# Kernel tuning notes

Hardware: AMD Instinct MI355X
Metric: run time of the kernel (lower is better)

## Reference

```python
import jax, jax.numpy as jnp
import numpy as np

K = 8  # avg_kernel (pool kernel == stride, and nearest-upsample factor)


def conv1x1(u, W, b):
    # 1x1 conv == per-pixel linear map over channels
    return jnp.einsum('bchw,oc->bohw', u, W) + b[None, :, None, None]


def setup_inputs() -> dict:
    key = jax.random.key(0)
    ks = jax.random.split(key, 9)
    C = 64
    x = jax.random.normal(ks[0], (8, C, 512, 512), dtype=jnp.float32)
    def w(k):
        return jax.random.normal(k, (C, C), dtype=jnp.float32) * 0.05
    def bias(k):
        return jax.random.normal(k, (C,), dtype=jnp.float32) * 0.05
    return {
        'x': x,
        'Wt': w(ks[1]), 'bt': bias(ks[2]),
        'Wp': w(ks[3]), 'bp': bias(ks[4]),
        'Wg': w(ks[5]), 'bg': bias(ks[6]),
        'Wc': w(ks[7]), 'bc': bias(ks[8]),
    }


def reference(x, Wt, bt, Wp, bp, Wg, bg, Wc, bc):
    B, C, H, W = x.shape
    # AvgPool2d(kernel=K, stride=K): exact reshape-mean since H,W divisible by K
    u = x.reshape(B, C, H // K, K, W // K, K).mean(axis=(3, 5))  # [B,C,h,w]
    b_, c_, h, w_ = u.shape
    N = h * w_
    theta = conv1x1(u, Wt, bt).reshape(B, C, N).transpose(0, 2, 1)  # [B,N,C]
    phi = conv1x1(u, Wp, bp).reshape(B, C, N)                       # [B,C,N] (downsample = flatten)
    g = conv1x1(u, Wg, bg).reshape(B, C, N).transpose(0, 2, 1)      # [B,N,C]
    attn = jax.nn.softmax(jnp.einsum('bnc,bcm->bnm', theta, phi), axis=-1)  # [B,N,N], unscaled
    y = jnp.einsum('bnm,bmc->bnc', attn, g)                         # [B,N,C]
    y = y.transpose(0, 2, 1).reshape(B, C, h, w_)
    y = conv1x1(y, Wc, bc)
    # F.interpolate(size=[H,W]) default nearest; integer factor K -> exact repeat
    y = jnp.repeat(jnp.repeat(y, K, axis=2), K, axis=3)
    return y
```

## Files before the change

kernel.cpp:

```cpp
#include <hip/hip_runtime.h>
#include <hip/hip_bf16.h>


typedef short short8 __attribute__((ext_vector_type(8)));
typedef float floatx4 __attribute__((ext_vector_type(4)));

__device__ inline unsigned short f2bf(float f) {
    union { float f; unsigned int u; } v; v.f = f;
    unsigned int u = v.u;
    u += 0x7fff + ((u >> 16) & 1);
    return (unsigned short)(u >> 16);
}

__device__ inline float rowsum16(float x) {
    x += __int_as_float(__builtin_amdgcn_update_dpp(0, __float_as_int(x), 0x121, 0xf, 0xf, false));
    x += __int_as_float(__builtin_amdgcn_update_dpp(0, __float_as_int(x), 0x122, 0xf, 0xf, false));
    x += __int_as_float(__builtin_amdgcn_update_dpp(0, __float_as_int(x), 0x124, 0xf, 0xf, false));
    x += __int_as_float(__builtin_amdgcn_update_dpp(0, __float_as_int(x), 0x128, 0xf, 0xf, false));
    return x;
}

__global__ __launch_bounds__(256) void k_pool(const float* __restrict__ x,
                                              float* __restrict__ u) {
    int id = blockIdx.x * 256 + threadIdx.x;
    int ow = id & 63;
    int oh = (id >> 6) & 63;
    int bc = id >> 12;
    const float* p = x + ((size_t)bc * 512 + oh * 8) * 512 + ow * 8;
    float s = 0.f;
#pragma unroll
    for (int r = 0; r < 8; ++r) {
        const float4* q = (const float4*)(p + r * 512);
        float4 a = q[0], b = q[1];
        s += a.x + a.y + a.z + a.w + b.x + b.y + b.z + b.w;
    }
    u[id] = s * (1.f / 64.f);
}

__global__ __launch_bounds__(256) void k_qkv(const float* __restrict__ u,
    const float* __restrict__ Wt, const float* __restrict__ bt,
    const float* __restrict__ Wp, const float* __restrict__ bp,
    const float* __restrict__ Wg, const float* __restrict__ bg,
    unsigned short* __restrict__ th, unsigned short* __restrict__ ph,
    unsigned short* __restrict__ gT) {
    __shared__ float U[64 * 68];
    int b = blockIdx.x >> 6;
    int n0 = (blockIdx.x & 63) * 64;
    int t = threadIdx.x;
    int lane = t & 63, wv = t >> 6;
#pragma unroll
    for (int i = 0; i < 4; ++i) {
        int f4 = t + 256 * i;
        int cin = f4 >> 4, pos = f4 & 15;
        float4 v = *(const float4*)(u + ((size_t)(b * 64 + cin)) * 4096 + n0 + pos * 4);
        U[(pos * 4 + 0) * 68 + cin] = v.x;
        U[(pos * 4 + 1) * 68 + cin] = v.y;
        U[(pos * 4 + 2) * 68 + cin] = v.z;
        U[(pos * 4 + 3) * 68 + cin] = v.w;
    }
    __syncthreads();
    float4 ur[16];
#pragma unroll
    for (int q = 0; q < 16; ++q) ur[q] = *(const float4*)&U[lane * 68 + q * 4];
    __syncthreads();
    unsigned* T = (unsigned*)U;
    int cb = __builtin_amdgcn_readfirstlane(wv * 16);
    size_t gbase = (size_t)(b * 64) * 4096 + n0 + lane;
    float atp = 0.f, app = 0.f;
#pragma unroll 2
    for (int i = 0; i < 16; ++i) {
        int cout = cb + i;
        const float* wt = Wt + cout * 64;
        const float* wp = Wp + cout * 64;
        const float* wg = Wg + cout * 64;
        float t0 = bt[cout], t1 = 0.f;
        float q0 = bp[cout], q1 = 0.f;
        float g0 = bg[cout], g1 = 0.f;
#pragma unroll
        for (int q = 0; q < 16; ++q) {
            float4 x = ur[q];
            if (q & 1) {
                t1 = fmaf(wt[4*q+3], x.w, fmaf(wt[4*q+2], x.z, fmaf(wt[4*q+1], x.y, fmaf(wt[4*q], x.x, t1))));
                q1 = fmaf(wp[4*q+3], x.w, fmaf(wp[4*q+2], x.z, fmaf(wp[4*q+1], x.y, fmaf(wp[4*q], x.x, q1))));
                g1 = fmaf(wg[4*q+3], x.w, fmaf(wg[4*q+2], x.z, fmaf(wg[4*q+1], x.y, fmaf(wg[4*q], x.x, g1))));
            } else {
                t0 = fmaf(wt[4*q+3], x.w, fmaf(wt[4*q+2], x.z, fmaf(wt[4*q+1], x.y, fmaf(wt[4*q], x.x, t0))));
                q0 = fmaf(wp[4*q+3], x.w, fmaf(wp[4*q+2], x.z, fmaf(wp[4*q+1], x.y, fmaf(wp[4*q], x.x, q0))));
                g0 = fmaf(wg[4*q+3], x.w, fmaf(wg[4*q+2], x.z, fmaf(wg[4*q+1], x.y, fmaf(wg[4*q], x.x, g0))));
            }
        }
        float at = t0 + t1, ap = q0 + q1, ag = g0 + g1;
        gT[gbase + (size_t)cout * 4096] = f2bf(ag);
        if (i & 1) {
            T[lane * 68 + wv * 8 + (i >> 1)]      = (unsigned)f2bf(atp) | ((unsigned)f2bf(at) << 16);
            T[lane * 68 + 32 + wv * 8 + (i >> 1)] = (unsigned)f2bf(app) | ((unsigned)f2bf(ap) << 16);
        } else { atp = at; app = ap; }
    }
    __syncthreads();
#pragma unroll
    for (int j = 0; j < 2; ++j) {
        int qi = t + 256 * j;
        int r = qi >> 3, c4 = qi & 7;
        uint4 vt = *(const uint4*)&T[r * 68 + c4 * 4];
        uint4 vp = *(const uint4*)&T[r * 68 + 32 + c4 * 4];
        size_t o = ((size_t)(b * 4096 + n0 + r)) * 64 + c4 * 8;
        *(uint4*)(th + o) = vt;
        *(uint4*)(ph + o) = vp;
    }
}

__global__ __launch_bounds__(256) void k_attn(
    const unsigned short* __restrict__ th,
    const unsigned short* __restrict__ ph,
    const unsigned short* __restrict__ gT,
    float* __restrict__ y) {
    __shared__ unsigned short Th[64 * 72];
    __shared__ unsigned short Ph[2][64 * 72];
    __shared__ unsigned short Gt[2][64 * 72];
    __shared__ unsigned short Pl[4 * 16 * 72];
    int b = blockIdx.x >> 6;
    int n0 = (blockIdx.x & 63) * 64;
    int t = threadIdx.x;
    int wave = t >> 6, lane = t & 63, quad = lane >> 4, l16 = lane & 15;
    int row = t >> 2, cg = t & 3;

    {
        const unsigned short* src = th + ((size_t)(b * 4096 + n0 + row)) * 64;
        *(short8*)(Th + row * 72 + cg * 8)      = *(const short8*)(src + cg * 8);
        *(short8*)(Th + row * 72 + 32 + cg * 8) = *(const short8*)(src + 32 + cg * 8);
        const unsigned short* sp = ph + ((size_t)(b * 4096 + row)) * 64;
        *(short8*)(Ph[0] + row * 72 + cg * 8)      = *(const short8*)(sp + cg * 8);
        *(short8*)(Ph[0] + row * 72 + 32 + cg * 8) = *(const short8*)(sp + 32 + cg * 8);
        const unsigned short* sg = gT + ((size_t)(b * 64 + row)) * 4096;
        *(short8*)(Gt[0] + row * 72 + cg * 8)      = *(const short8*)(sg + cg * 8);
        *(short8*)(Gt[0] + row * 72 + 32 + cg * 8) = *(const short8*)(sg + 32 + cg * 8);
    }
    __syncthreads();
    short8 a0 = *(const short8*)(Th + (wave * 16 + l16) * 72 + quad * 8);
    short8 a1 = *(const short8*)(Th + (wave * 16 + l16) * 72 + 32 + quad * 8);

    floatx4 Yacc[4];
#pragma unroll
    for (int ct = 0; ct < 4; ++ct) Yacc[ct] = (floatx4){0.f, 0.f, 0.f, 0.f};
    float l[4] = {0.f, 0.f, 0.f, 0.f};

    int cur = 0;
    for (int mt = 0; mt < 64; ++mt) {
        int mn = ((mt + 1) & 63) * 64;
        short8 r0, r1, r2, r3;
        {
            const unsigned short* sp = ph + ((size_t)(b * 4096 + mn + row)) * 64;
            r0 = *(const short8*)(sp + cg * 8);
            r1 = *(const short8*)(sp + 32 + cg * 8);
            const unsigned short* sg = gT + ((size_t)(b * 64 + row)) * 4096 + mn;
            r2 = *(const short8*)(sg + cg * 8);
            r3 = *(const short8*)(sg + 32 + cg * 8);
        }
        const unsigned short* PhC = Ph[cur];
        const unsigned short* GtC = Gt[cur];

        float psum[4] = {0.f, 0.f, 0.f, 0.f};
#pragma unroll
        for (int ct = 0; ct < 4; ++ct) {
            short8 b0 = *(const short8*)(PhC + (ct * 16 + l16) * 72 + quad * 8);
            short8 b1 = *(const short8*)(PhC + (ct * 16 + l16) * 72 + 32 + quad * 8);
            floatx4 acc = (floatx4){0.f, 0.f, 0.f, 0.f};
            __builtin_amdgcn_s_setprio(1);
            acc = __builtin_amdgcn_mfma_f32_16x16x32_bf16(a0, b0, acc, 0, 0, 0);
            acc = __builtin_amdgcn_mfma_f32_16x16x32_bf16(a1, b1, acc, 0, 0, 0);
            __builtin_amdgcn_s_setprio(0);
#pragma unroll
            for (int r = 0; r < 4; ++r) {
                float e = __expf(acc[r]);
                psum[r] += e;
                Pl[wave * 16 * 72 + (quad * 4 + r) * 72 + ct * 16 + l16] = f2bf(e);
            }
        }
#pragma unroll
        for (int r = 0; r < 4; ++r) l[r] += rowsum16(psum[r]);
        short8 p0 = *(const short8*)(Pl + wave * 16 * 72 + l16 * 72 + quad * 8);
        short8 p1 = *(const short8*)(Pl + wave * 16 * 72 + l16 * 72 + 32 + quad * 8);
        __builtin_amdgcn_s_setprio(1);
#pragma unroll
        for (int ct = 0; ct < 4; ++ct) {
            short8 g0 = *(const short8*)(GtC + (ct * 16 + l16) * 72 + quad * 8);
            short8 g1 = *(const short8*)(GtC + (ct * 16 + l16) * 72 + 32 + quad * 8);
            Yacc[ct] = __builtin_amdgcn_mfma_f32_16x16x32_bf16(p0, g0, Yacc[ct], 0, 0, 0);
            Yacc[ct] = __builtin_amdgcn_mfma_f32_16x16x32_bf16(p1, g1, Yacc[ct], 0, 0, 0);
        }
        __builtin_amdgcn_s_setprio(0);
        unsigned short* PhN = Ph[cur ^ 1];
        unsigned short* GtN = Gt[cur ^ 1];
        *(short8*)(PhN + row * 72 + cg * 8)      = r0;
        *(short8*)(PhN + row * 72 + 32 + cg * 8) = r1;
        *(short8*)(GtN + row * 72 + cg * 8)      = r2;
        *(short8*)(GtN + row * 72 + 32 + cg * 8) = r3;
        __syncthreads();
        cur ^= 1;
    }
#pragma unroll
    for (int ct = 0; ct < 4; ++ct)
#pragma unroll
        for (int r = 0; r < 4; ++r) {
            int rr = n0 + wave * 16 + quad * 4 + r;
            y[((size_t)(b * 4096 + rr)) * 64 + ct * 16 + l16] = Yacc[ct][r] / l[r];
        }
}

__global__ __launch_bounds__(256) void k_out(const float* __restrict__ y,
    const float* __restrict__ Wc, const float* __restrict__ bc,
    float* __restrict__ out) {
    __shared__ float Y[64 * 66];
    int b = blockIdx.x >> 6;
    int oh = blockIdx.x & 63;
    int t = threadIdx.x;
#pragma unroll
    for (int i = 0; i < 4; ++i) {
        int f4 = t + 256 * i;
        int w = f4 >> 4, cgp = f4 & 15;
        float4 v = *(const float4*)(y + ((size_t)(b * 4096 + oh * 64 + w)) * 64 + cgp * 4);
        Y[(cgp * 4 + 0) * 66 + w] = v.x;
        Y[(cgp * 4 + 1) * 66 + w] = v.y;
        Y[(cgp * 4 + 2) * 66 + w] = v.z;
        Y[(cgp * 4 + 3) * 66 + w] = v.w;
    }
    __syncthreads();
    int w = t & 63, wv = t >> 6;
#pragma unroll 2
    for (int i = 0; i < 16; ++i) {
        int c = wv + 4 * i;
        float acc = bc[c];
#pragma unroll
        for (int cin = 0; cin < 64; ++cin)
            acc += Wc[c * 64 + cin] * Y[cin * 66 + w];
        float4 v4 = {acc, acc, acc, acc};
        float* base = out + (((size_t)(b * 64 + c)) * 512 + oh * 8) * 512 + w * 8;
#pragma unroll
        for (int r = 0; r < 8; ++r) {
            *(float4*)(base + (size_t)r * 512) = v4;
            *(float4*)(base + (size_t)r * 512 + 4) = v4;
        }
    }
}

extern "C" void kernel_launch(void* const* d_in, const int* in_sizes, int n_in,
                              void* d_out, int out_size, void* d_ws, size_t ws_size,
                              hipStream_t stream) {
    const float* x  = (const float*)d_in[0];
    const float* Wt = (const float*)d_in[1];
    const float* bt = (const float*)d_in[2];
    const float* Wp = (const float*)d_in[3];
    const float* bp = (const float*)d_in[4];
    const float* Wg = (const float*)d_in[5];
    const float* bg = (const float*)d_in[6];
    const float* Wc = (const float*)d_in[7];
    const float* bc = (const float*)d_in[8];
    float* out = (float*)d_out;
    char* ws = (char*)d_ws;
    float* u            = (float*)(ws);
    unsigned short* th  = (unsigned short*)(ws + (8  << 20));
    unsigned short* ph  = (unsigned short*)(ws + (12 << 20));
    unsigned short* gT  = (unsigned short*)(ws + (16 << 20));
    float* y            = (float*)(ws + (20 << 20));

    hipLaunchKernelGGL(k_pool, dim3(8192), dim3(256), 0, stream, x, u);
    hipLaunchKernelGGL(k_qkv,  dim3(512),  dim3(256), 0, stream,
                       u, Wt, bt, Wp, bp, Wg, bg, th, ph, gT);
    hipLaunchKernelGGL(k_attn, dim3(512),  dim3(256), 0, stream, th, ph, gT, y);
    hipLaunchKernelGGL(k_out,  dim3(512),  dim3(256), 0, stream, y, Wc, bc, out);
}
```

Measured before the change: 1.234 ms.

## Double attention query rows per block to reuse K/V tiles across two row groups

Each attention block now handles 128 query rows instead of 64, with each wave owning two 16-row groups that share the same phi/g LDS tiles. Theta fragments are loaded directly from global into registers, removing the Th shared buffer. This halves the number of K/V tile loads and barriers per query row, but it also halves the grid to 256 blocks, which may leave some of the MI355X's compute units idle, and it raises register use.

```diff
diff --git a/kernel.cpp b/kernel.cpp
--- a/kernel.cpp
+++ b/kernel.cpp
@@ -114,20 +114,23 @@
     const unsigned short* __restrict__ ph,
     const unsigned short* __restrict__ gT,
     float* __restrict__ y) {
-    __shared__ unsigned short Th[64 * 72];
     __shared__ unsigned short Ph[2][64 * 72];
     __shared__ unsigned short Gt[2][64 * 72];
-    __shared__ unsigned short Pl[4 * 16 * 72];
-    int b = blockIdx.x >> 6;
-    int n0 = (blockIdx.x & 63) * 64;
+    __shared__ unsigned short Pl[4][32 * 72];
+    int b = blockIdx.x >> 5;
+    int n0 = (blockIdx.x & 31) * 128;
     int t = threadIdx.x;
     int wave = t >> 6, lane = t & 63, quad = lane >> 4, l16 = lane & 15;
     int row = t >> 2, cg = t & 3;
 
+    short8 a[2][2];
+#pragma unroll
+    for (int rg = 0; rg < 2; ++rg) {
+        const unsigned short* src = th + ((size_t)(b * 4096 + n0 + wave * 32 + rg * 16 + l16)) * 64;
+        a[rg][0] = *(const short8*)(src + quad * 8);
+        a[rg][1] = *(const short8*)(src + 32 + quad * 8);
+    }
     {
-        const unsigned short* src = th + ((size_t)(b * 4096 + n0 + row)) * 64;
-        *(short8*)(Th + row * 72 + cg * 8)      = *(const short8*)(src + cg * 8);
-        *(short8*)(Th + row * 72 + 32 + cg * 8) = *(const short8*)(src + 32 + cg * 8);
         const unsigned short* sp = ph + ((size_t)(b * 4096 + row)) * 64;
         *(short8*)(Ph[0] + row * 72 + cg * 8)      = *(const short8*)(sp + cg * 8);
         *(short8*)(Ph[0] + row * 72 + 32 + cg * 8) = *(const short8*)(sp + 32 + cg * 8);
@@ -136,13 +139,13 @@
         *(short8*)(Gt[0] + row * 72 + 32 + cg * 8) = *(const short8*)(sg + 32 + cg * 8);
     }
     __syncthreads();
-    short8 a0 = *(const short8*)(Th + (wave * 16 + l16) * 72 + quad * 8);
-    short8 a1 = *(const short8*)(Th + (wave * 16 + l16) * 72 + 32 + quad * 8);
-
-    floatx4 Yacc[4];
-#pragma unroll
-    for (int ct = 0; ct < 4; ++ct) Yacc[ct] = (floatx4){0.f, 0.f, 0.f, 0.f};
-    float l[4] = {0.f, 0.f, 0.f, 0.f};
+
+    floatx4 Yacc[2][4];
+#pragma unroll
+    for (int rg = 0; rg < 2; ++rg)
+#pragma unroll
+        for (int ct = 0; ct < 4; ++ct) Yacc[rg][ct] = (floatx4){0.f, 0.f, 0.f, 0.f};
+    float l[2][4] = {{0.f,0.f,0.f,0.f},{0.f,0.f,0.f,0.f}};
 
     int cur = 0;
     for (int mt = 0; mt < 64; ++mt) {
@@ -159,34 +162,46 @@
         const unsigned short* PhC = Ph[cur];
         const unsigned short* GtC = Gt[cur];
 
-        float psum[4] = {0.f, 0.f, 0.f, 0.f};
+        float psum[2][4] = {{0.f,0.f,0.f,0.f},{0.f,0.f,0.f,0.f}};
 #pragma unroll
         for (int ct = 0; ct < 4; ++ct) {
             short8 b0 = *(const short8*)(PhC + (ct * 16 + l16) * 72 + quad * 8);
             short8 b1 = *(const short8*)(PhC + (ct * 16 + l16) * 72 + 32 + quad * 8);
-            floatx4 acc = (floatx4){0.f, 0.f, 0.f, 0.f};
-            __builtin_amdgcn_s_setprio(1);
-            acc = __builtin_amdgcn_mfma_f32_16x16x32_bf16(a0, b0, acc, 0, 0, 0);
-            acc = __builtin_amdgcn_mfma_f32_16x16x32_bf16(a1, b1, acc, 0, 0, 0);
-            __builtin_amdgcn_s_setprio(0);
-#pragma unroll
-            for (int r = 0; r < 4; ++r) {
-                float e = __expf(acc[r]);
-                psum[r] += e;
-                Pl[wave * 16 * 72 + (quad * 4 + r) * 72 + ct * 16 + l16] = f2bf(e);
-            }
-        }
-#pragma unroll
-        for (int r = 0; r < 4; ++r) l[r] += rowsum16(psum[r]);
-        short8 p0 = *(const short8*)(Pl + wave * 16 * 72 + l16 * 72 + quad * 8);
-        short8 p1 = *(const short8*)(Pl + wave * 16 * 72 + l16 * 72 + 32 + quad * 8);
+#pragma unroll
+            for (int rg = 0; rg < 2; ++rg) {
+                floatx4 acc = (floatx4){0.f, 0.f, 0.f, 0.f};
+                __builtin_amdgcn_s_setprio(1);
+                acc = __builtin_amdgcn_mfma_f32_16x16x32_bf16(a[rg][0], b0, acc, 0, 0, 0);
+                acc = __builtin_amdgcn_mfma_f32_16x16x32_bf16(a[rg][1], b1, acc, 0, 0, 0);
+                __builtin_amdgcn_s_setprio(0);
+#pragma unroll
+                for (int r = 0; r < 4; ++r) {
+                    float e = __expf(acc[r]);
+                    psum[rg][r] += e;
+                    Pl[wave][(rg * 16 + quad * 4 + r) * 72 + ct * 16 + l16] = f2bf(e);
+                }
+            }
+        }
+#pragma unroll
+        for (int rg = 0; rg < 2; ++rg)
+#pragma unroll
+            for (int r = 0; r < 4; ++r) l[rg][r] += rowsum16(psum[rg][r]);
+        short8 p[2][2];
+#pragma unroll
+        for (int rg = 0; rg < 2; ++rg) {
+            p[rg][0] = *(const short8*)(Pl[wave] + (rg * 16 + l16) * 72 + quad * 8);
+            p[rg][1] = *(const short8*)(Pl[wave] + (rg * 16 + l16) * 72 + 32 + quad * 8);
+        }
         __builtin_amdgcn_s_setprio(1);
 #pragma unroll
         for (int ct = 0; ct < 4; ++ct) {
             short8 g0 = *(const short8*)(GtC + (ct * 16 + l16) * 72 + quad * 8);
             short8 g1 = *(const short8*)(GtC + (ct * 16 + l16) * 72 + 32 + quad * 8);
-            Yacc[ct] = __builtin_amdgcn_mfma_f32_16x16x32_bf16(p0, g0, Yacc[ct], 0, 0, 0);
-            Yacc[ct] = __builtin_amdgcn_mfma_f32_16x16x32_bf16(p1, g1, Yacc[ct], 0, 0, 0);
+#pragma unroll
+            for (int rg = 0; rg < 2; ++rg) {
+                Yacc[rg][ct] = __builtin_amdgcn_mfma_f32_16x16x32_bf16(p[rg][0], g0, Yacc[rg][ct], 0, 0, 0);
+                Yacc[rg][ct] = __builtin_amdgcn_mfma_f32_16x16x32_bf16(p[rg][1], g1, Yacc[rg][ct], 0, 0, 0);
+            }
         }
         __builtin_amdgcn_s_setprio(0);
         unsigned short* PhN = Ph[cur ^ 1];
@@ -199,12 +214,14 @@
         cur ^= 1;
     }
 #pragma unroll
-    for (int ct = 0; ct < 4; ++ct)
-#pragma unroll
-        for (int r = 0; r < 4; ++r) {
-            int rr = n0 + wave * 16 + quad * 4 + r;
-            y[((size_t)(b * 4096 + rr)) * 64 + ct * 16 + l16] = Yacc[ct][r] / l[r];
-        }
+    for (int rg = 0; rg < 2; ++rg)
+#pragma unroll
+        for (int ct = 0; ct < 4; ++ct)
+#pragma unroll
+            for (int r = 0; r < 4; ++r) {
+                int rr = n0 + wave * 32 + rg * 16 + quad * 4 + r;
+                y[((size_t)(b * 4096 + rr)) * 64 + ct * 16 + l16] = Yacc[rg][ct][r] / l[rg][r];
+            }
 }
 
 __global__ __launch_bounds__(256) void k_out(const float* __restrict__ y,
@@ -266,6 +283,6 @@
     hipLaunchKernelGGL(k_pool, dim3(8192), dim3(256), 0, stream, x, u);
     hipLaunchKernelGGL(k_qkv,  dim3(512),  dim3(256), 0, stream,
                        u, Wt, bt, Wp, bp, Wg, bg, th, ph, gT);
-    hipLaunchKernelGGL(k_attn, dim3(512),  dim3(256), 0, stream, th, ph, gT, y);
+    hipLaunchKernelGGL(k_attn, dim3(256),  dim3(256), 0, stream, th, ph, gT, y);
     hipLaunchKernelGGL(k_out,  dim3(512),  dim3(256), 0, stream, y, Wc, bc, out);
 }
```

Measured after the change: 1.248 ms. About the same (+1.1%).
